# Optimization experiments

Hardware: AMD Instinct MI355X
Metric: run time of the kernel (lower is better)

Reference implementation:

```python
import jax, jax.numpy as jnp
import numpy as np

H, DK, DV, SEG, D = 16, 64, 64, 512, 1024


def setup_inputs() -> dict:
    key = jax.random.key(0)
    ks = jax.random.split(key, 6)
    B, T = 2, 8192
    x = jax.random.normal(ks[0], (B, T, D), jnp.float32)
    Wq = jax.random.normal(ks[1], (H * DK, D), jnp.float32) * 0.02
    Wk = jax.random.normal(ks[2], (H * DK, D), jnp.float32) * 0.02
    Wv = jax.random.normal(ks[3], (H * DV, D), jnp.float32) * 0.02
    Wout = jax.random.normal(ks[4], (D, H * DV), jnp.float32) * 0.02
    betas = jax.random.normal(ks[5], (1, H, 1, DV), jnp.float32)
    return {"x": x, "Wq": Wq, "Wk": Wk, "Wv": Wv, "Wout": Wout, "betas": betas}


def reference(x, Wq, Wk, Wv, Wout, betas):
    B, T, _ = x.shape
    n_seg = T // SEG
    # Projections for the whole sequence, then PyTorch-style .view head split:
    # per segment, (B, SEG, H*dk).view(B, H, SEG, dk) is a raw row-major reshape.
    q = (x @ Wq.T).reshape(B, n_seg, H, SEG, DK)
    k = (x @ Wk.T).reshape(B, n_seg, H, SEG, DK)
    v = (x @ Wv.T).reshape(B, n_seg, H, SEG, DV)
    qs = jnp.moveaxis(q, 1, 0)  # (n_seg, B, H, SEG, DK)
    ks_ = jnp.moveaxis(k, 1, 0)
    vs = jnp.moveaxis(v, 1, 0)

    gate = jax.nn.sigmoid(betas)                 # (1, H, 1, DV)
    scale = 1.0 / jnp.sqrt(jnp.float32(DK))

    mem0 = jnp.zeros((B, H, DK, DV), x.dtype)
    # z broadcasts from (B,H,DV,1) to (B,H,DV,DK) on first update; start dense.
    z0 = jnp.zeros((B, H, DV, DK), x.dtype)

    def step(carry, seg):
        mem, z = carry
        q, k, v = seg
        sq = jax.nn.elu(q) + 1.0                 # (B,H,S,DK)
        sk = jax.nn.elu(k) + 1.0
        z = z + sk.sum(axis=-2, keepdims=True)   # (B,H,DV,DK) via broadcast
        scores = jnp.einsum('bhsd,bhtd->bhst', q, k) * scale
        att_dot = jnp.einsum('bhst,bhtv->bhsv', jax.nn.softmax(scores, axis=-1), v)
        att_mem = jnp.einsum('bhsd,bhdv->bhsv', sq, mem) / jnp.einsum('bhsd,bhdv->bhsv', sq, z)
        mem = mem + jnp.einsum('bhsd,bhsv->bhdv', sk, v)  # linear update (after att_mem)
        att = gate * att_mem + (1.0 - gate) * att_dot     # (B,H,S,DV)
        # PyTorch .view(B, SEG, H*DV) on (B,H,S,DV): raw reshape, no transpose.
        y = att.reshape(B, SEG, H * DV) @ Wout.T          # (B,SEG,D)
        return (mem, z), y

    (_, _), ys = jax.lax.scan(step, (mem0, z0), (qs, ks_, vs))
    out = jnp.moveaxis(ys, 0, 1).reshape(B, T, D)
    return out
```

## Files before the change

kernel.cpp:

```cpp
#include <hip/hip_runtime.h>


#define H_ 16
#define SEG_ 512
#define NSEG_ 16
#define B_ 2
#define T_ 8192
#define D_ 1024
#define BT_ 16384

#define NPROJ ((size_t)BT_ * D_)
#define NW ((size_t)D_ * D_)

__device__ unsigned short g_qb[NPROJ], g_kb[NPROJ], g_vb[NPROJ];
__device__ unsigned short g_xh[NPROJ];
__device__ unsigned short g_wqkv[3 * NW];
__device__ unsigned short g_ath[NPROJ], g_atl[NPROJ];
__device__ unsigned short g_woh[NW], g_wol[NW];
__device__ unsigned short g_vt[(size_t)512 * 64 * 512];
__device__ float g_M[(size_t)512 * 4096];
__device__ float g_z[(size_t)512 * 64];

typedef __attribute__((ext_vector_type(8))) short short8;
typedef __attribute__((ext_vector_type(8))) unsigned short ushort8;
typedef __attribute__((ext_vector_type(4))) float f32x4;

__device__ __forceinline__ float elu1(float x) {
    return x > 0.f ? x + 1.f : __expf(x);
}
__device__ __forceinline__ unsigned short f2bf(float x) {
    unsigned u = __float_as_uint(x);
    u += 0x7fffu + ((u >> 16) & 1u);
    return (unsigned short)(u >> 16);
}
__device__ __forceinline__ float bf2f(unsigned short h) {
    return __uint_as_float((unsigned)h << 16);
}
__device__ __forceinline__ void load_lds16(const unsigned short* g, unsigned short* l) {
    __builtin_amdgcn_global_load_lds(
        (const __attribute__((address_space(1))) unsigned int*)g,
        (__attribute__((address_space(3))) unsigned int*)l, 16, 0, 0);
}
__device__ __forceinline__ int sz8(int row, int blk) {
    return row * 64 + ((blk ^ (row & 7)) << 3);
}

__global__ __launch_bounds__(256) void cast_bf16(
    const float* __restrict__ in, unsigned short* __restrict__ out, int n)
{
    int i = (blockIdx.x * 256 + threadIdx.x) * 4;
    if (i >= n) return;
    float4 x = *(const float4*)(in + i);
    ushort4 h;
    h.x = f2bf(x.x); h.y = f2bf(x.y); h.z = f2bf(x.z); h.w = f2bf(x.w);
    *(ushort4*)(out + i) = h;
}

__global__ __launch_bounds__(256) void split_bf16(
    const float* __restrict__ in, unsigned short* __restrict__ hi,
    unsigned short* __restrict__ lo, int n)
{
    int i = (blockIdx.x * 256 + threadIdx.x) * 4;
    if (i >= n) return;
    float4 x = *(const float4*)(in + i);
    ushort4 h, l;
    h.x = f2bf(x.x); l.x = f2bf(x.x - bf2f(h.x));
    h.y = f2bf(x.y); l.y = f2bf(x.y - bf2f(h.y));
    h.z = f2bf(x.z); l.z = f2bf(x.z - bf2f(h.z));
    h.w = f2bf(x.w); l.w = f2bf(x.w - bf2f(h.w));
    *(ushort4*)(hi + i) = h;
    *(ushort4*)(lo + i) = l;
}


#define VMC(N) asm volatile("s_waitcnt vmcnt(" #N ")" ::: "memory")

#define STAGE_A(p, h, tt, u) \
    load_lds16(Aw + ((h) * 128 + (u) * 8) * 1024 + (tt) * 64, \
               &lds[(p) * 32768 + ((h) * 128 + w * 16 + (u) * 8) * 64])
#define STAGE_B(p, h, tt, u) \
    load_lds16(Bww + ((h) * 128 + (u) * 8) * 1024 + (tt) * 64, \
               &lds[(p) * 32768 + 16384 + ((h) * 128 + w * 16 + (u) * 8) * 64])
#define STAGE_AH(p, h, tt) do { STAGE_A(p, h, tt, 0); STAGE_A(p, h, tt, 1); } while (0)
#define STAGE_BH(p, h, tt) do { STAGE_B(p, h, tt, 0); STAGE_B(p, h, tt, 1); } while (0)

#define LDA(PBUF, MLO) do { \
    _Pragma("unroll") for (int m2 = 0; m2 < 4; ++m2) \
    _Pragma("unroll") for (int ks2 = 0; ks2 < 2; ++ks2) \
        a[m2][ks2] = *(const short8*)&lds[(PBUF) * 32768 + aoff[ks2] + ((MLO) + m2) * 1024]; \
} while (0)

#define LDB(PBUF) do { \
    _Pragma("unroll") for (int n2 = 0; n2 < 4; ++n2) \
    _Pragma("unroll") for (int ks2 = 0; ks2 < 2; ++ks2) \
        b[n2][ks2] = *(const short8*)&lds[(PBUF) * 32768 + boff[ks2] + n2 * 1024]; \
} while (0)

#define MFMA_QUAD(MLO, NLO) do { \
    _Pragma("unroll") for (int m2 = 0; m2 < 4; ++m2) \
    _Pragma("unroll") for (int n2 = 0; n2 < 2; ++n2) \
    _Pragma("unroll") for (int ks2 = 0; ks2 < 2; ++ks2) \
        acc[(MLO) + m2][(NLO) + n2] = __builtin_amdgcn_mfma_f32_16x16x32_bf16( \
            a[m2][ks2], b[(NLO) + n2][ks2], acc[(MLO) + m2][(NLO) + n2], 0, 0, 0); \
} while (0)

#define PH(MLO, NLO) do { \
    __builtin_amdgcn_s_barrier(); \
    asm volatile("s_waitcnt lgkmcnt(0)" ::: "memory"); \
    __builtin_amdgcn_sched_barrier(0); \
    __builtin_amdgcn_s_setprio(1); \
    MFMA_QUAD(MLO, NLO); \
    __builtin_amdgcn_s_setprio(0); \
    __builtin_amdgcn_sched_barrier(0); \
    __builtin_amdgcn_s_barrier(); \
} while (0)

__global__ __launch_bounds__(512, 2) void gemm_qkv8(
    const unsigned short* __restrict__ A, const unsigned short* __restrict__ Bw,
    unsigned short* __restrict__ Q, unsigned short* __restrict__ Kp,
    unsigned short* __restrict__ V)
{
    __shared__ unsigned short lds[65536];
    const int t = threadIdx.x, lane = t & 63, w = t >> 6;
    const int wave_m = w >> 2, wave_n = w & 3;

    const int bid = blockIdx.x;
    const int sb = (bid & 7) * 96 + (bid >> 3);
    const int mb = sb / 12, nb = sb % 12;
    const int m0 = mb * 256, n0 = nb * 256;

    const int lrow = lane >> 3;
    const int lcol = ((lane & 7) ^ lrow) * 8;
    const unsigned short* Aw  = A  + (size_t)(m0 + w * 16 + lrow) * 1024 + lcol;
    const unsigned short* Bww = Bw + (size_t)(n0 + w * 16 + lrow) * 1024 + lcol;

    const int fr = lane & 15, g4 = lane >> 4;
    int aoff[2], boff[2];
#pragma unroll
    for (int ks2 = 0; ks2 < 2; ++ks2) {
        aoff[ks2] = (wave_m * 128 + fr) * 64 + (((ks2 * 4 + g4) ^ (fr & 7)) * 8);
        boff[ks2] = 16384 + (wave_n * 64 + fr) * 64 + (((ks2 * 4 + g4) ^ (fr & 7)) * 8);
    }

    f32x4 acc[8][4];
#pragma unroll
    for (int i = 0; i < 8; ++i)
#pragma unroll
        for (int j = 0; j < 4; ++j) acc[i][j] = (f32x4)0.f;
    short8 a[4][2], b[4][2];

    STAGE_BH(0, 0, 0); STAGE_BH(0, 1, 0); STAGE_AH(0, 0, 0); STAGE_AH(0, 1, 0);
    STAGE_BH(1, 0, 1); STAGE_BH(1, 1, 1); STAGE_AH(1, 0, 1);
    VMC(6);
    __builtin_amdgcn_s_barrier();

#pragma unroll 1
    for (int it = 0; it < 7; ++it) {
        const int t1 = 2 * it + 1, t2 = 2 * it + 2, t3 = 2 * it + 3;
        LDB(0); LDA(0, 0);
        STAGE_AH(1, 1, t1);
        PH(0, 0);
        STAGE_BH(0, 0, t2);
        PH(0, 2);
        LDA(0, 4);
        STAGE_BH(0, 1, t2);
        PH(4, 0);
        STAGE_AH(0, 0, t2);
        VMC(6);
        PH(4, 2);
        LDB(1); LDA(1, 0);
        STAGE_AH(0, 1, t2);
        PH(0, 0);
        STAGE_BH(1, 0, t3);
        PH(0, 2);
        LDA(1, 4);
        STAGE_BH(1, 1, t3);
        PH(4, 0);
        STAGE_AH(1, 0, t3);
        VMC(6);
        PH(4, 2);
    }
    LDB(0); LDA(0, 0);
    STAGE_AH(1, 1, 15);
    PH(0, 0);
    PH(0, 2);
    LDA(0, 4);
    PH(4, 0);
    VMC(0);
    PH(4, 2);
    LDB(1); LDA(1, 0);
    PH(0, 0);
    PH(0, 2);
    LDA(1, 4);
    PH(4, 0);
    PH(4, 2);

    const int ccol = lane & 15, crow = (lane >> 4) * 4;
#pragma unroll
    for (int m = 0; m < 8; ++m)
#pragma unroll
        for (int n = 0; n < 4; ++n) {
            const int row = wave_m * 128 + m * 16 + crow;
            const int col = wave_n * 64 + n * 16 + ccol;
#pragma unroll
            for (int r = 0; r < 4; ++r)
                lds[(row + r) * 256 + col] = f2bf(acc[m][n][r]);
        }
    __syncthreads();
    const int which = n0 >> 10, col0 = n0 & 1023;
    unsigned short* outp = which == 0 ? Q : (which == 1 ? Kp : V);
    const int orow = t >> 1, och = (t & 1) * 128;
    unsigned short* gp = outp + (size_t)(m0 + orow) * 1024 + col0 + och;
    const unsigned short* lp = &lds[orow * 256 + och];
#pragma unroll
    for (int u = 0; u < 128; u += 8)
        *(ushort8*)(gp + u) = *(const ushort8*)(lp + u);
}


#define OSTG(p, arrp, aroff, tt, u) \
    load_lds16(arrp + (size_t)(u) * 16 * 1024 + (tt) * 32, \
               &lds[(p) * 32768 + (aroff) + (w * 32 + (u) * 16) * 32])
#define OUNIT(p, arrp, aroff, tt) do { OSTG(p, arrp, aroff, tt, 0); OSTG(p, arrp, aroff, tt, 1); } while (0)

#define OLDA(PBUF, MLO) do { \
    _Pragma("unroll") for (int m2 = 0; m2 < 4; ++m2) { \
        ah[m2] = *(const short8*)&lds[(PBUF) * 32768 +         ao + ((MLO) + m2) * 512]; \
        al[m2] = *(const short8*)&lds[(PBUF) * 32768 +  8192 + ao + ((MLO) + m2) * 512]; \
    } \
} while (0)

#define OLDB(PBUF) do { \
    _Pragma("unroll") for (int n2 = 0; n2 < 4; ++n2) { \
        bh[n2] = *(const short8*)&lds[(PBUF) * 32768 + 16384 + bo + n2 * 512]; \
        bl[n2] = *(const short8*)&lds[(PBUF) * 32768 + 24576 + bo + n2 * 512]; \
    } \
} while (0)

#define OQUAD(MLO, NLO) do { \
    _Pragma("unroll") for (int m2 = 0; m2 < 4; ++m2) \
    _Pragma("unroll") for (int n2 = 0; n2 < 2; ++n2) { \
        acc[(MLO) + m2][(NLO) + n2] = __builtin_amdgcn_mfma_f32_16x16x32_bf16( \
            ah[m2], bh[(NLO) + n2], acc[(MLO) + m2][(NLO) + n2], 0, 0, 0); \
        acc[(MLO) + m2][(NLO) + n2] = __builtin_amdgcn_mfma_f32_16x16x32_bf16( \
            al[m2], bh[(NLO) + n2], acc[(MLO) + m2][(NLO) + n2], 0, 0, 0); \
        acc[(MLO) + m2][(NLO) + n2] = __builtin_amdgcn_mfma_f32_16x16x32_bf16( \
            ah[m2], bl[(NLO) + n2], acc[(MLO) + m2][(NLO) + n2], 0, 0, 0); \
    } \
} while (0)

#define OPH(MLO, NLO) do { \
    __builtin_amdgcn_s_barrier(); \
    asm volatile("s_waitcnt lgkmcnt(0)" ::: "memory"); \
    __builtin_amdgcn_sched_barrier(0); \
    __builtin_amdgcn_s_setprio(1); \
    OQUAD(MLO, NLO); \
    __builtin_amdgcn_s_setprio(0); \
    __builtin_amdgcn_sched_barrier(0); \
    __builtin_amdgcn_s_barrier(); \
} while (0)

__global__ __launch_bounds__(512, 2) void gemm_bt8(
    const unsigned short* __restrict__ Ah, const unsigned short* __restrict__ Al,
    const unsigned short* __restrict__ Bh, const unsigned short* __restrict__ Bl,
    float* __restrict__ C)
{
    __shared__ unsigned short lds[65536];
    const int t = threadIdx.x, lane = t & 63, w = t >> 6;
    const int wave_m = w >> 2, wave_n = w & 3;

    const int bid = blockIdx.x;
    const int sb = (bid & 7) * 32 + (bid >> 3);
    const int m0 = (sb >> 2) * 256, n0 = (sb & 3) * 256;

    const int lrow = lane >> 2;
    const int lcol = ((lane & 3) ^ ((lane >> 3) & 3)) * 8;
    const unsigned short* Ahp = Ah + (size_t)(m0 + w * 32 + lrow) * 1024 + lcol;
    const unsigned short* Alp = Al + (size_t)(m0 + w * 32 + lrow) * 1024 + lcol;
    const unsigned short* Bhp = Bh + (size_t)(n0 + w * 32 + lrow) * 1024 + lcol;
    const unsigned short* Blp = Bl + (size_t)(n0 + w * 32 + lrow) * 1024 + lcol;

    const int fr = lane & 15, g4 = lane >> 4;
    const int xo = (g4 ^ ((fr >> 1) & 3)) * 8;
    const int ao = (wave_m * 128 + fr) * 32 + xo;
    const int bo = (wave_n * 64 + fr) * 32 + xo;

    f32x4 acc[8][4];
#pragma unroll
    for (int i = 0; i < 8; ++i)
#pragma unroll
        for (int j = 0; j < 4; ++j) acc[i][j] = (f32x4)0.f;
    short8 ah[4], al[4], bh[4], bl[4];

    OUNIT(0, Bhp, 16384, 0); OUNIT(0, Blp, 24576, 0); OUNIT(0, Ahp, 0, 0); OUNIT(0, Alp, 8192, 0);
    OUNIT(1, Bhp, 16384, 1); OUNIT(1, Blp, 24576, 1); OUNIT(1, Ahp, 0, 1);
    VMC(6);
    __builtin_amdgcn_s_barrier();

#pragma unroll 1
    for (int it = 0; it < 15; ++it) {
        const int t1 = 2 * it + 1, t2 = 2 * it + 2, t3 = 2 * it + 3;
        OLDB(0); OLDA(0, 0);
        OUNIT(1, Alp, 8192, t1);
        OPH(0, 0);
        OUNIT(0, Bhp, 16384, t2);
        OPH(0, 2);
        OLDA(0, 4);
        OUNIT(0, Blp, 24576, t2);
        OPH(4, 0);
        OUNIT(0, Ahp, 0, t2);
        VMC(6);
        OPH(4, 2);
        OLDB(1); OLDA(1, 0);
        OUNIT(0, Alp, 8192, t2);
        OPH(0, 0);
        OUNIT(1, Bhp, 16384, t3);
        OPH(0, 2);
        OLDA(1, 4);
        OUNIT(1, Blp, 24576, t3);
        OPH(4, 0);
        OUNIT(1, Ahp, 0, t3);
        VMC(6);
        OPH(4, 2);
    }
    OLDB(0); OLDA(0, 0);
    OUNIT(1, Alp, 8192, 31);
    OPH(0, 0);
    OPH(0, 2);
    OLDA(0, 4);
    OPH(4, 0);
    VMC(0);
    OPH(4, 2);
    OLDB(1); OLDA(1, 0);
    OPH(0, 0);
    OPH(0, 2);
    OLDA(1, 4);
    OPH(4, 0);
    OPH(4, 2);

    const int ccol = lane & 15, crow = (lane >> 4) * 4;
#pragma unroll
    for (int m = 0; m < 8; ++m)
#pragma unroll
        for (int n = 0; n < 4; ++n) {
            float* cp = C + (size_t)(m0 + wave_m * 128 + m * 16 + crow) * 1024
                          + (n0 + wave_n * 64 + n * 16 + ccol);
#pragma unroll
            for (int r = 0; r < 4; ++r) cp[(size_t)r * 1024] = acc[m][n][r];
        }
}

__global__ __launch_bounds__(256) void seg_stats(
    const unsigned short* __restrict__ kproj, const unsigned short* __restrict__ vproj,
    float* __restrict__ Mseg, float* __restrict__ zsum,
    unsigned short* __restrict__ vtg)
{
    __shared__ float ks[64][68];
    __shared__ float vs[64][68];
    const int idx = blockIdx.x;
    const int seg = idx & 15;
    const int bh  = idx >> 4;
    const int h   = bh & 15;
    const int b   = bh >> 4;
    const size_t base = ((size_t)b * T_ + (size_t)seg * SEG_ + (size_t)h * 32) * D_;
    const unsigned short* kt = kproj + base;
    const unsigned short* vt = vproj + base;
    const int t  = threadIdx.x;
    const int d0 = (t >> 4) * 4;
    const int v0 = (t & 15) * 4;
    const int lr = t >> 2;
    const int lc = (t & 3) * 16;
    float acc[4][4];
#pragma unroll
    for (int i = 0; i < 4; ++i)
#pragma unroll
        for (int j = 0; j < 4; ++j) acc[i][j] = 0.f;
    float zacc = 0.f;

    for (int c0 = 0; c0 < SEG_; c0 += 64) {
        __syncthreads();
        {
            const unsigned short* kp = kt + (size_t)(c0 + lr) * 64 + lc;
            const unsigned short* vp = vt + (size_t)(c0 + lr) * 64 + lc;
            ushort8 k0 = *(const ushort8*)kp,       k1 = *(const ushort8*)(kp + 8);
            ushort8 v0v = *(const ushort8*)vp,      v1 = *(const ushort8*)(vp + 8);
#pragma unroll
            for (int e = 0; e < 8; ++e) {
                ks[lr][lc + e]     = elu1(bf2f(k0[e]));
                ks[lr][lc + 8 + e] = elu1(bf2f(k1[e]));
                vs[lr][lc + e]     = bf2f(v0v[e]);
                vs[lr][lc + 8 + e] = bf2f(v1[e]);
            }
        }
        __syncthreads();
#pragma unroll 8
        for (int i = 0; i < 64; ++i) {
            float a0 = ks[i][d0 + 0], a1 = ks[i][d0 + 1];
            float a2 = ks[i][d0 + 2], a3 = ks[i][d0 + 3];
            float b0 = vs[i][v0 + 0], b1 = vs[i][v0 + 1];
            float b2 = vs[i][v0 + 2], b3 = vs[i][v0 + 3];
            acc[0][0] += a0 * b0; acc[0][1] += a0 * b1; acc[0][2] += a0 * b2; acc[0][3] += a0 * b3;
            acc[1][0] += a1 * b0; acc[1][1] += a1 * b1; acc[1][2] += a1 * b2; acc[1][3] += a1 * b3;
            acc[2][0] += a2 * b0; acc[2][1] += a2 * b1; acc[2][2] += a2 * b2; acc[2][3] += a2 * b3;
            acc[3][0] += a3 * b0; acc[3][1] += a3 * b1; acc[3][2] += a3 * b2; acc[3][3] += a3 * b3;
        }
        if (t < 64) {
#pragma unroll 8
            for (int i = 0; i < 64; ++i) zacc += ks[i][t];
        }
        {
            ushort8 w0, w1;
#pragma unroll
            for (int i = 0; i < 8; ++i) w0[i] = f2bf(vs[lc + i][lr]);
#pragma unroll
            for (int i = 0; i < 8; ++i) w1[i] = f2bf(vs[lc + 8 + i][lr]);
            unsigned short* vo = vtg + ((size_t)idx * 64 + lr) * 512 + c0 + lc;
            *(ushort8*)vo       = w0;
            *(ushort8*)(vo + 8) = w1;
        }
    }
    float* Mout = Mseg + (size_t)idx * 4096;
#pragma unroll
    for (int i = 0; i < 4; ++i)
        *(float4*)(Mout + (size_t)(d0 + i) * 64 + v0) =
            make_float4(acc[i][0], acc[i][1], acc[i][2], acc[i][3]);
    if (t < 64) zsum[(size_t)idx * 64 + t] = zacc;
}

__global__ __launch_bounds__(256) void prefix_scan(
    float* __restrict__ M, float* __restrict__ z)
{
    const int bh = blockIdx.x;
    const int t  = threadIdx.x;
    float run[16];
#pragma unroll
    for (int u = 0; u < 16; ++u) run[u] = 0.f;
    float runz = 0.f;
    for (int seg = 0; seg < NSEG_; ++seg) {
        const size_t o = ((size_t)bh * NSEG_ + seg) * 4096 + (size_t)t * 16;
#pragma unroll
        for (int u = 0; u < 16; u += 4) {
            float4 m = *(const float4*)(M + o + u);
            *(float4*)(M + o + u) = make_float4(run[u], run[u+1], run[u+2], run[u+3]);
            run[u] += m.x; run[u+1] += m.y; run[u+2] += m.z; run[u+3] += m.w;
        }
        if (t < 64) {
            const size_t oz = ((size_t)bh * NSEG_ + seg) * 64 + t;
            runz += z[oz];
            z[oz] = runz;
        }
    }
}

__global__ __launch_bounds__(256) void attn_mfma(
    const unsigned short* __restrict__ qproj, const unsigned short* __restrict__ kproj,
    const unsigned short* __restrict__ vtg, const float* __restrict__ memb,
    const float* __restrict__ Zaf, const float* __restrict__ betas,
    unsigned short* __restrict__ ath, unsigned short* __restrict__ atl)
{
    __shared__ unsigned short sm_k[64 * 64];
    __shared__ unsigned short sm_v[64 * 64];
    __shared__ unsigned short sm_p[64 * 64];
    __shared__ float Zsh[64], gsh[64];

    const int idx  = blockIdx.x;
    const int qc   = (idx >> 3) & 7;
    const int rest = (idx >> 6) * 8 + (idx & 7);
    const int bh   = rest >> 4;
    const int seg  = rest & 15;
    const int h    = bh & 15;
    const int b    = bh >> 4;
    const size_t base = ((size_t)b * T_ + (size_t)seg * SEG_ + (size_t)h * 32) * D_;

    const int t    = threadIdx.x;
    const int lane = t & 63;
    const int w    = t >> 6;
    const int c16  = lane & 15;
    const int g4   = lane >> 4;
    const int lr   = t >> 2;
    const int lc   = (t & 3) * 16;

    const unsigned short* qt = qproj + base + (size_t)qc * 4096;
    const unsigned short* kt = kproj + base;
    const unsigned short* vt = vtg + (size_t)rest * (64 * 512);
    const float* mb = memb + (size_t)rest * 4096;

    if (t < 64) {
        Zsh[t] = Zaf[(size_t)rest * 64 + t];
        gsh[t] = 1.f / (1.f + __expf(-betas[h * 64 + t]));
    }

    short8 qh[2], sqh[2];
    float rowsum = 0.f;
#pragma unroll
    for (int ks = 0; ks < 2; ++ks) {
        const unsigned short* qp = qt + (size_t)(w * 16 + c16) * 64 + g4 * 8 + ks * 32;
        ushort8 qv = *(const ushort8*)qp;
        short8 qf, sf;
#pragma unroll
        for (int j = 0; j < 8; ++j) {
            float e = elu1(bf2f(qv[j]));
            rowsum += e;
            qf[j] = (short)qv[j];
            sf[j] = (short)f2bf(e);
        }
        qh[ks] = qf; sqh[ks] = sf;
    }
    rowsum += __shfl_xor(rowsum, 16);
    rowsum += __shfl_xor(rowsum, 32);

    {
        const float* mp = mb + (size_t)lr * 64 + lc;
#pragma unroll
        for (int u = 0; u < 4; ++u) {
            float4 m4 = *(const float4*)(mp + u * 4);
            sm_p[sz8(lc + u * 4 + 0, lr >> 3) + (lr & 7)] = f2bf(m4.x);
            sm_p[sz8(lc + u * 4 + 1, lr >> 3) + (lr & 7)] = f2bf(m4.y);
            sm_p[sz8(lc + u * 4 + 2, lr >> 3) + (lr & 7)] = f2bf(m4.z);
            sm_p[sz8(lc + u * 4 + 3, lr >> 3) + (lr & 7)] = f2bf(m4.w);
        }
    }
    __syncthreads();

    f32x4 numf[4];
#pragma unroll
    for (int nf = 0; nf < 4; ++nf) numf[nf] = (f32x4)0.f;
#pragma unroll
    for (int ks = 0; ks < 2; ++ks)
#pragma unroll
        for (int nf = 0; nf < 4; ++nf) {
            short8 bm = *(const short8*)&sm_p[sz8(nf * 16 + c16, g4 + ks * 4)];
            numf[nf] = __builtin_amdgcn_mfma_f32_16x16x32_bf16(sqh[ks], bm, numf[nf], 0, 0, 0);
        }

    short8 bones;
#pragma unroll
    for (int j = 0; j < 8; ++j) bones[j] = (short)0x3F80;

    f32x4 o[4];
#pragma unroll
    for (int nf = 0; nf < 4; ++nf) o[nf] = (f32x4)0.f;
    float mrow[4] = {-1e30f, -1e30f, -1e30f, -1e30f};
    float lrow[4] = {0.f, 0.f, 0.f, 0.f};

    for (int kb = 0; kb < 8; ++kb) {
        __syncthreads();
        {
            const unsigned short* kp = kt + (size_t)(kb * 64 + lr) * 64 + lc;
            *(ushort8*)&sm_k[sz8(lr, lc >> 3)]       = *(const ushort8*)kp;
            *(ushort8*)&sm_k[sz8(lr, (lc >> 3) + 1)] = *(const ushort8*)(kp + 8);
            const unsigned short* vp = vt + (size_t)lr * 512 + kb * 64 + lc;
            *(ushort8*)&sm_v[sz8(lr, lc >> 3)]       = *(const ushort8*)vp;
            *(ushort8*)&sm_v[sz8(lr, (lc >> 3) + 1)] = *(const ushort8*)(vp + 8);
        }
        __syncthreads();

        f32x4 s[4];
#pragma unroll
        for (int nf = 0; nf < 4; ++nf) s[nf] = (f32x4)0.f;
#pragma unroll
        for (int ks = 0; ks < 2; ++ks)
#pragma unroll
            for (int nf = 0; nf < 4; ++nf) {
                short8 bk = *(const short8*)&sm_k[sz8(nf * 16 + c16, g4 + ks * 4)];
                s[nf] = __builtin_amdgcn_mfma_f32_16x16x32_bf16(qh[ks], bk, s[nf], 0, 0, 0);
            }
#pragma unroll
        for (int nf = 0; nf < 4; ++nf) s[nf] *= 0.125f;

        float pmax[4];
#pragma unroll
        for (int r = 0; r < 4; ++r)
            pmax[r] = fmaxf(fmaxf(s[0][r], s[1][r]), fmaxf(s[2][r], s[3][r]));
        const bool ok = pmax[0] <= mrow[0] + 8.f && pmax[1] <= mrow[1] + 8.f &&
                        pmax[2] <= mrow[2] + 8.f && pmax[3] <= mrow[3] + 8.f;
        if (!__all(ok)) {
#pragma unroll
            for (int r = 0; r < 4; ++r) {
                float mx = pmax[r];
                mx = fmaxf(mx, __shfl_xor(mx, 1));
                mx = fmaxf(mx, __shfl_xor(mx, 2));
                mx = fmaxf(mx, __shfl_xor(mx, 4));
                mx = fmaxf(mx, __shfl_xor(mx, 8));
                const float mnew = fmaxf(mrow[r], mx);
                const float corr = __expf(mrow[r] - mnew);
                mrow[r] = mnew;
                lrow[r] *= corr;
#pragma unroll
                for (int nf = 0; nf < 4; ++nf) o[nf][r] *= corr;
            }
        }
#pragma unroll
        for (int nf = 0; nf < 4; ++nf)
#pragma unroll
            for (int r = 0; r < 4; ++r) {
                s[nf][r] = __expf(s[nf][r] - mrow[r]);
                sm_p[sz8(w * 16 + g4 * 4 + r, nf * 2 + (c16 >> 3)) + (c16 & 7)] =
                    f2bf(s[nf][r]);
            }

        f32x4 psum = (f32x4)0.f;
#pragma unroll
        for (int ks = 0; ks < 2; ++ks) {
            short8 pa = *(const short8*)&sm_p[sz8(w * 16 + c16, g4 + ks * 4)];
            psum = __builtin_amdgcn_mfma_f32_16x16x32_bf16(pa, bones, psum, 0, 0, 0);
#pragma unroll
            for (int nf = 0; nf < 4; ++nf) {
                short8 bv = *(const short8*)&sm_v[sz8(nf * 16 + c16, g4 + ks * 4)];
                o[nf] = __builtin_amdgcn_mfma_f32_16x16x32_bf16(pa, bv, o[nf], 0, 0, 0);
            }
        }
#pragma unroll
        for (int r = 0; r < 4; ++r) lrow[r] += psum[r];
    }

    __syncthreads();

    float rs[4], invl[4];
#pragma unroll
    for (int r = 0; r < 4; ++r) {
        rs[r]   = __shfl(rowsum, (g4 << 2) + r);
        invl[r] = 1.f / lrow[r];
    }
#pragma unroll
    for (int nf = 0; nf < 4; ++nf) {
        const int col = nf * 16 + c16;
        const float Zc = Zsh[col], gc = gsh[col];
        const float izc = 1.f / Zc;
#pragma unroll
        for (int r = 0; r < 4; ++r) {
            const float adot = o[nf][r] * invl[r];
            const float amem = numf[nf][r] * izc / rs[r];
            const float res  = gc * amem + (1.f - gc) * adot;
            const unsigned short hv = f2bf(res);
            const unsigned short lv = f2bf(res - bf2f(hv));
            const int row = w * 16 + g4 * 4 + r;
            const int so  = sz8(row, nf * 2 + (c16 >> 3)) + (c16 & 7);
            sm_k[so] = hv;
            sm_v[so] = lv;
        }
    }
    __syncthreads();
    {
        const size_t ob = base + (size_t)(qc * 64 + lr) * 64 + lc;
        *(ushort8*)(ath + ob)     = *(const ushort8*)&sm_k[sz8(lr, lc >> 3)];
        *(ushort8*)(ath + ob + 8) = *(const ushort8*)&sm_k[sz8(lr, (lc >> 3) + 1)];
        *(ushort8*)(atl + ob)     = *(const ushort8*)&sm_v[sz8(lr, lc >> 3)];
        *(ushort8*)(atl + ob + 8) = *(const ushort8*)&sm_v[sz8(lr, (lc >> 3) + 1)];
    }
}

extern "C" void kernel_launch(void* const* d_in, const int* in_sizes, int n_in,
                              void* d_out, int out_size, void* d_ws, size_t ws_size,
                              hipStream_t stream) {
    const float* x     = (const float*)d_in[0];
    const float* Wq    = (const float*)d_in[1];
    const float* Wk    = (const float*)d_in[2];
    const float* Wv    = (const float*)d_in[3];
    const float* Wout  = (const float*)d_in[4];
    const float* betas = (const float*)d_in[5];
    float* out = (float*)d_out;
    (void)d_ws; (void)ws_size;

    float *M, *z;
    unsigned short *qb, *kb, *vb, *xh, *wqkv, *vt, *ath, *atl, *woh, *wol;
    hipGetSymbolAddress((void**)&qb,   HIP_SYMBOL(g_qb));
    hipGetSymbolAddress((void**)&kb,   HIP_SYMBOL(g_kb));
    hipGetSymbolAddress((void**)&vb,   HIP_SYMBOL(g_vb));
    hipGetSymbolAddress((void**)&xh,   HIP_SYMBOL(g_xh));
    hipGetSymbolAddress((void**)&wqkv, HIP_SYMBOL(g_wqkv));
    hipGetSymbolAddress((void**)&vt,   HIP_SYMBOL(g_vt));
    hipGetSymbolAddress((void**)&ath,  HIP_SYMBOL(g_ath));
    hipGetSymbolAddress((void**)&atl,  HIP_SYMBOL(g_atl));
    hipGetSymbolAddress((void**)&woh,  HIP_SYMBOL(g_woh));
    hipGetSymbolAddress((void**)&wol,  HIP_SYMBOL(g_wol));
    hipGetSymbolAddress((void**)&M,    HIP_SYMBOL(g_M));
    hipGetSymbolAddress((void**)&z,    HIP_SYMBOL(g_z));

    const int nX = (int)NPROJ, nW = (int)NW;
    cast_bf16<<<nX / 1024, 256, 0, stream>>>(x, xh, nX);
    cast_bf16<<<nW / 1024, 256, 0, stream>>>(Wq, wqkv, nW);
    cast_bf16<<<nW / 1024, 256, 0, stream>>>(Wk, wqkv + NW, nW);
    cast_bf16<<<nW / 1024, 256, 0, stream>>>(Wv, wqkv + 2 * NW, nW);
    split_bf16<<<nW / 1024, 256, 0, stream>>>(Wout, woh, wol, nW);

    gemm_qkv8<<<dim3(768), 512, 0, stream>>>(xh, wqkv, qb, kb, vb);
    seg_stats<<<B_ * H_ * NSEG_, 256, 0, stream>>>(kb, vb, M, z, vt);
    prefix_scan<<<B_ * H_, 256, 0, stream>>>(M, z);
    attn_mfma<<<B_ * H_ * NSEG_ * 8, 256, 0, stream>>>(qb, kb, vt, M, z, betas, ath, atl);
    gemm_bt8<<<dim3(256), 512, 0, stream>>>(ath, atl, woh, wol, out);
}
```

Before: 512.2 us.

## Fuse cast kernels, swizzle QKV epilogue LDS, widen prefix scan grid

Merges the five separate bf16 cast/split launches into a single prep kernel to cut launch overhead. Adds an XOR swizzle to the QKV GEMM epilogue's LDS staging to reduce bank conflicts on the row-strided writes. Splits the prefix scan across four blocks per batch-head, so 128 blocks instead of 32 each carry a float4 running sum, which raises parallelism for the serial scan. The added block-index branching is small, but the swizzle indexing must match exactly on the write and read sides.

```diff
diff --git a/kernel.cpp b/kernel.cpp
--- a/kernel.cpp
+++ b/kernel.cpp
@@ -45,31 +45,45 @@
     return row * 64 + ((blk ^ (row & 7)) << 3);
 }
 
-__global__ __launch_bounds__(256) void cast_bf16(
-    const float* __restrict__ in, unsigned short* __restrict__ out, int n)
+__global__ __launch_bounds__(256) void prep_cast(
+    const float* __restrict__ x, const float* __restrict__ Wq,
+    const float* __restrict__ Wk, const float* __restrict__ Wv,
+    const float* __restrict__ Wout,
+    unsigned short* __restrict__ xh, unsigned short* __restrict__ wqkv,
+    unsigned short* __restrict__ woh, unsigned short* __restrict__ wol)
 {
-    int i = (blockIdx.x * 256 + threadIdx.x) * 4;
-    if (i >= n) return;
-    float4 x = *(const float4*)(in + i);
-    ushort4 h;
-    h.x = f2bf(x.x); h.y = f2bf(x.y); h.z = f2bf(x.z); h.w = f2bf(x.w);
-    *(ushort4*)(out + i) = h;
-}
-
-__global__ __launch_bounds__(256) void split_bf16(
-    const float* __restrict__ in, unsigned short* __restrict__ hi,
-    unsigned short* __restrict__ lo, int n)
-{
-    int i = (blockIdx.x * 256 + threadIdx.x) * 4;
-    if (i >= n) return;
-    float4 x = *(const float4*)(in + i);
-    ushort4 h, l;
-    h.x = f2bf(x.x); l.x = f2bf(x.x - bf2f(h.x));
-    h.y = f2bf(x.y); l.y = f2bf(x.y - bf2f(h.y));
-    h.z = f2bf(x.z); l.z = f2bf(x.z - bf2f(h.z));
-    h.w = f2bf(x.w); l.w = f2bf(x.w - bf2f(h.w));
-    *(ushort4*)(hi + i) = h;
-    *(ushort4*)(lo + i) = l;
+    const int b = blockIdx.x;
+    const int nXB = (int)(NPROJ / 1024);
+    const int nWB = (int)(NW / 1024);
+    if (b < nXB + 3 * nWB) {
+        const float* in;
+        unsigned short* out;
+        int i;
+        if (b < nXB) {
+            in = x; out = xh; i = (b * 256 + threadIdx.x) * 4;
+        } else {
+            const int wsel = (b - nXB) / nWB;
+            const int wb   = (b - nXB) % nWB;
+            in  = wsel == 0 ? Wq : (wsel == 1 ? Wk : Wv);
+            out = wqkv + (size_t)wsel * NW;
+            i = (wb * 256 + threadIdx.x) * 4;
+        }
+        float4 v = *(const float4*)(in + i);
+        ushort4 h;
+        h.x = f2bf(v.x); h.y = f2bf(v.y); h.z = f2bf(v.z); h.w = f2bf(v.w);
+        *(ushort4*)(out + i) = h;
+    } else {
+        const int wb = b - nXB - 3 * nWB;
+        const int i = (wb * 256 + threadIdx.x) * 4;
+        float4 v = *(const float4*)(Wout + i);
+        ushort4 h, l;
+        h.x = f2bf(v.x); l.x = f2bf(v.x - bf2f(h.x));
+        h.y = f2bf(v.y); l.y = f2bf(v.y - bf2f(h.y));
+        h.z = f2bf(v.z); l.z = f2bf(v.z - bf2f(h.z));
+        h.w = f2bf(v.w); l.w = f2bf(v.w - bf2f(h.w));
+        *(ushort4*)(woh + i) = h;
+        *(ushort4*)(wol + i) = l;
+    }
 }
 
 
@@ -200,21 +214,24 @@
     for (int m = 0; m < 8; ++m)
 #pragma unroll
         for (int n = 0; n < 4; ++n) {
-            const int row = wave_m * 128 + m * 16 + crow;
             const int col = wave_n * 64 + n * 16 + ccol;
-#pragma unroll
-            for (int r = 0; r < 4; ++r)
-                lds[(row + r) * 256 + col] = f2bf(acc[m][n][r]);
+            const int cb = col >> 3, cl = col & 7;
+#pragma unroll
+            for (int r = 0; r < 4; ++r) {
+                const int row = wave_m * 128 + m * 16 + crow + r;
+                lds[row * 256 + ((cb ^ (row & 31)) << 3) + cl] = f2bf(acc[m][n][r]);
+            }
         }
     __syncthreads();
     const int which = n0 >> 10, col0 = n0 & 1023;
     unsigned short* outp = which == 0 ? Q : (which == 1 ? Kp : V);
     const int orow = t >> 1, och = (t & 1) * 128;
     unsigned short* gp = outp + (size_t)(m0 + orow) * 1024 + col0 + och;
-    const unsigned short* lp = &lds[orow * 256 + och];
-#pragma unroll
-    for (int u = 0; u < 128; u += 8)
-        *(ushort8*)(gp + u) = *(const ushort8*)(lp + u);
+#pragma unroll
+    for (int u = 0; u < 128; u += 8) {
+        const int bo = (och + u) >> 3;
+        *(ushort8*)(gp + u) = *(const ushort8*)&lds[orow * 256 + ((bo ^ (orow & 31)) << 3)];
+    }
 }
 
 
@@ -430,21 +447,18 @@
 __global__ __launch_bounds__(256) void prefix_scan(
     float* __restrict__ M, float* __restrict__ z)
 {
-    const int bh = blockIdx.x;
-    const int t  = threadIdx.x;
-    float run[16];
-#pragma unroll
-    for (int u = 0; u < 16; ++u) run[u] = 0.f;
+    const int blk = blockIdx.x;
+    const int bh  = blk >> 2, sl = blk & 3;
+    const int t   = threadIdx.x;
+    const size_t off = (size_t)bh * NSEG_ * 4096 + (size_t)sl * 1024 + (size_t)t * 4;
+    float4 run = make_float4(0.f, 0.f, 0.f, 0.f);
     float runz = 0.f;
     for (int seg = 0; seg < NSEG_; ++seg) {
-        const size_t o = ((size_t)bh * NSEG_ + seg) * 4096 + (size_t)t * 16;
-#pragma unroll
-        for (int u = 0; u < 16; u += 4) {
-            float4 m = *(const float4*)(M + o + u);
-            *(float4*)(M + o + u) = make_float4(run[u], run[u+1], run[u+2], run[u+3]);
-            run[u] += m.x; run[u+1] += m.y; run[u+2] += m.z; run[u+3] += m.w;
-        }
-        if (t < 64) {
+        const size_t o = off + (size_t)seg * 4096;
+        float4 m = *(const float4*)(M + o);
+        *(float4*)(M + o) = run;
+        run.x += m.x; run.y += m.y; run.z += m.z; run.w += m.w;
+        if (sl == 0 && t < 64) {
             const size_t oz = ((size_t)bh * NSEG_ + seg) * 64 + t;
             runz += z[oz];
             z[oz] = runz;
@@ -677,16 +691,13 @@
     hipGetSymbolAddress((void**)&M,    HIP_SYMBOL(g_M));
     hipGetSymbolAddress((void**)&z,    HIP_SYMBOL(g_z));
 
-    const int nX = (int)NPROJ, nW = (int)NW;
-    cast_bf16<<<nX / 1024, 256, 0, stream>>>(x, xh, nX);
-    cast_bf16<<<nW / 1024, 256, 0, stream>>>(Wq, wqkv, nW);
-    cast_bf16<<<nW / 1024, 256, 0, stream>>>(Wk, wqkv + NW, nW);
-    cast_bf16<<<nW / 1024, 256, 0, stream>>>(Wv, wqkv + 2 * NW, nW);
-    split_bf16<<<nW / 1024, 256, 0, stream>>>(Wout, woh, wol, nW);
+    const int nXB = (int)(NPROJ / 1024), nWB = (int)(NW / 1024);
+    prep_cast<<<nXB + 4 * nWB, 256, 0, stream>>>(x, Wq, Wk, Wv, Wout,
+                                                 xh, wqkv, woh, wol);
 
     gemm_qkv8<<<dim3(768), 512, 0, stream>>>(xh, wqkv, qb, kb, vb);
     seg_stats<<<B_ * H_ * NSEG_, 256, 0, stream>>>(kb, vb, M, z, vt);
-    prefix_scan<<<B_ * H_, 256, 0, stream>>>(M, z);
+    prefix_scan<<<B_ * H_ * 4, 256, 0, stream>>>(M, z);
     attn_mfma<<<B_ * H_ * NSEG_ * 8, 256, 0, stream>>>(qb, kb, vt, M, z, betas, ath, atl);
     gemm_bt8<<<dim3(256), 512, 0, stream>>>(ath, atl, woh, wol, out);
 }
```

Measured after the change: 502.4 us. About the same (-1.9%).
